# Kernel tuning notes

Hardware: AMD Instinct MI355X
Metric: run time of the kernel (lower is better)

The kernel has to match this reference:

```python
import jax, jax.numpy as jnp
import numpy as np

B, N, DIM, H, DH = 2, 1024, 1024, 8, 64
DI = H * DH  # 512
K = 4        # depthwise conv kernel
EPS = 1.1920929e-07  # float32 eps (torch RMSNorm default)


def setup_inputs() -> dict:
    key = jax.random.key(0)
    ks = jax.random.split(key, 12)
    s = lambda k, shape, sc=0.02: jax.random.normal(k, shape, jnp.float32) * sc
    return dict(
        x=jax.random.normal(ks[0], (B, N, DIM), jnp.float32),
        w_rms=jnp.ones((DIM,), jnp.float32),
        wq=s(ks[1], (DIM, DI)), wk=s(ks[2], (DIM, DI)), wv=s(ks[3], (DIM, DI)),
        wo=s(ks[4], (DI, DIM)),
        conv_q=s(ks[5], (DIM, K), 0.3), conv_k=s(ks[6], (DIM, K), 0.3), conv_v=s(ks[7], (DIM, K), 0.3),
        gamma_q=jnp.ones((H, 1, DH), jnp.float32), gamma_k=jnp.ones((H, 1, DH), jnp.float32),
        lr_w=s(ks[8], (DIM, H)), lr_b=jnp.full((H,), -4.0, jnp.float32),
        decay_w=s(ks[9], (DIM, H)), decay_b=jnp.full((H,), 4.0, jnp.float32),
        mom_w=s(ks[10], (DIM, H)), mom_b=jnp.full((H,), 2.0, jnp.float32),
    )


def rmsnorm(x, w):
    return x * jax.lax.rsqrt(jnp.mean(x * x, -1, keepdims=True) + EPS) * w


def mh_rmsnorm(x, gamma):  # x: (b, h, n, d)
    rms = jnp.sqrt(jnp.sum(x * x, -1, keepdims=True)) * (DH ** -0.5)
    return x / jnp.maximum(rms, 1e-8) * gamma


def dwconv(x, w):  # x: (b, n, dim), w: (dim, K) depthwise, padding K//2 -> length n+1
    y = jax.lax.conv_general_dilated(
        x.transpose(0, 2, 1), w[:, None, :], (1,), [(K // 2, K // 2)],
        feature_group_count=DIM, dimension_numbers=('NCW', 'OIW', 'NCW'))
    return y.transpose(0, 2, 1)


def gated_scan(a, x):  # h_t = a_t h_{t-1} + x_t, h_{-1}=0; a:(bh,t), x:(bh,t,d,d)
    def combine(c1, c2):
        a1, x1 = c1
        a2, x2 = c2
        return a1 * a2, a2 * x1 + x2
    _, h = jax.lax.associative_scan(combine, (a[..., None, None], x), axis=1)
    return h


def reference(x, w_rms, wq, wk, wv, wo, conv_q, conv_k, conv_v,
              gamma_q, gamma_k, lr_w, lr_b, decay_w, decay_b, mom_w, mom_b):
    b, n, _ = x.shape
    xa = rmsnorm(x, w_rms)
    qi, ki, vi = dwconv(xa, conv_q), dwconv(xa, conv_k), dwconv(xa, conv_v)
    split = lambda t: t.reshape(b, -1, H, DH).transpose(0, 2, 1, 3)[:, :, :n]  # (b,h,n,d)
    q = mh_rmsnorm(split(qi @ wq), gamma_q)
    k = mh_rmsnorm(split(ki @ wk), gamma_k)
    v = split(vi @ wv)
    fq = q.reshape(b * H, n, DH)
    fk = k.reshape(b * H, n, DH)
    fv = v.reshape(b * H, n, DH)
    sig = jax.nn.sigmoid
    lr = sig(xa @ lr_w + lr_b).transpose(0, 2, 1).reshape(b * H, n)
    decay = sig(xa @ decay_w + decay_b).transpose(0, 2, 1).reshape(b * H, n)
    mom = sig(xa @ mom_w + mom_b).transpose(0, 2, 1).reshape(b * H, n)
    # S_ref = S0 = 0 (fresh state) => pred = 0, delta_vec = -v
    g = jnp.einsum('bti,btj->btij', -fv, fk)          # (bh, n, d, d)
    Z = gated_scan(mom, g)                             # momentum scan
    S = gated_scan(decay, -lr[..., None, None] * Z)    # memory scan
    S_prev = jnp.concatenate([jnp.zeros_like(S[:, :1]), S[:, :-1]], axis=1)
    y = jnp.einsum('btdp,btp->btd', S_prev, fq)        # retrieval y_t = S_{t-1} psi_t
    y = y.reshape(b, H, n, DH).transpose(0, 2, 1, 3).reshape(b, n, DI)
    return y @ wo
```

## Files before the change

kernel.cpp:

```cpp
#include <hip/hip_runtime.h>
#include <math.h>

#define DEV __device__ __forceinline__

constexpr int Bb   = 2;
constexpr int Seq  = 1024;
constexpr int Dim  = 1024;
constexpr int Hh   = 8;
constexpr int Dh   = 64;
constexpr int Di   = 512;
constexpr int BN   = Bb * Seq;
constexpr int NSEQ = Bb * Hh;
constexpr int CHUNK = 32;
constexpr int CLEN  = Seq / CHUNK;
constexpr float EPSV = 1.1920929e-07f;
constexpr int NT2  = 8;
constexpr int KSPL = 8;

typedef _Float16 half8 __attribute__((ext_vector_type(8)));
typedef float    f32x4 __attribute__((ext_vector_type(4)));

DEV float bf2f(unsigned short u) {
  union { unsigned int i; float f; } x; x.i = ((unsigned int)u) << 16; return x.f;
}
DEV unsigned short f2bf(float f) {
  union { float f; unsigned int i; } x; x.f = f;
  unsigned int r = x.i + 0x7fffu + ((x.i >> 16) & 1u);
  return (unsigned short)(r >> 16);
}
DEV float ldin(const void* p, int f32, size_t i) {
  if (f32) return ((const float*)p)[i];
  return bf2f(((const unsigned short*)p)[i]);
}
DEV void ld4(const void* p, int f32, size_t i, float* dst) {
  if (f32) {
    float4 u = *(const float4*)((const float*)p + i);
    dst[0] = u.x; dst[1] = u.y; dst[2] = u.z; dst[3] = u.w;
  } else {
    ushort4 u = *(const ushort4*)((const unsigned short*)p + i);
    dst[0] = bf2f(u.x); dst[1] = bf2f(u.y); dst[2] = bf2f(u.z); dst[3] = bf2f(u.w);
  }
}
DEV int sniff_vote(const void* p, int n, int tid) {
  int j = 2 * tid, valid = 0, bad = 0;
  if (j < n) {
    valid = 1;
    float v = bf2f(((const unsigned short*)p)[j]);
    float a = fabsf(v);
    if (!(a >= 1e-12f && a <= 1e4f)) bad = 1;
  }
#pragma unroll
  for (int m = 1; m < 64; m <<= 1) { valid += __shfl_xor(valid, m); bad += __shfl_xor(bad, m); }
  return (2 * bad > valid) ? 1 : 0;
}

DEV void gld16(const _Float16* g, _Float16* l) {
  __builtin_amdgcn_global_load_lds(
      (const __attribute__((address_space(1))) void*)g,
      (__attribute__((address_space(3))) void*)l, 16, 0, 0);
}

struct InPtrs { const void* p[17]; int n[17]; };

__global__ __launch_bounds__(256) void k_front(
    InPtrs ip,
    int* __restrict__ flags,
    _Float16* __restrict__ wqT, _Float16* __restrict__ wkT,
    _Float16* __restrict__ wvT, _Float16* __restrict__ woT,
    _Float16* __restrict__ WgT,
    float* __restrict__ gqf, float* __restrict__ gkf, float* __restrict__ gbf,
    _Float16* __restrict__ xaf,
    _Float16* __restrict__ qc, _Float16* __restrict__ kc,
    _Float16* __restrict__ vc)
{
  int blk = blockIdx.x;
  int tid = threadIdx.x;
  __shared__ int sfl[8];
  __shared__ __align__(16) char smem_u[11 * Dim * 2];

  if (blk < 1024) {
    int z = blk >> 8, bx = blk & 15, by = (blk >> 4) & 15;
    int idx = (z == 0) ? 2 : ((z == 1) ? 3 : ((z == 2) ? 4 : 5));
    const void* src = ip.p[idx];
    _Float16* dst   = (z == 0) ? wqT : ((z == 1) ? wkT : ((z == 2) ? wvT : woT));
    int Kd = (z < 3) ? Dim : Di;
    int Nn = (z < 3) ? Di : Dim;
    int n0 = bx * 64, k0 = by * 64;
    if (n0 >= Nn || k0 >= Kd) return;

    if (tid < 64) { int f = sniff_vote(src, ip.n[idx], tid); if (tid == 0) sfl[0] = f; }
    __syncthreads();
    int f = sfl[0];

    float (*tile)[65] = (float(*)[65])smem_u;
    int r = tid >> 4, c4 = (tid & 15) * 4;
#pragma unroll
    for (int rr = 0; rr < 4; ++rr) {
      int k = rr * 16 + r;
      ld4(src, f, (size_t)(k0 + k) * Nn + n0 + c4, &tile[k][c4]);
    }
    __syncthreads();
#pragma unroll
    for (int rr = 0; rr < 4; ++rr) {
      int n = rr * 16 + r;
      _Float16 o4[4];
#pragma unroll
      for (int j = 0; j < 4; ++j) o4[j] = (_Float16)tile[c4 + j][n];
      *(ushort4*)&dst[(size_t)(n0 + n) * Kd + k0 + c4] = *(ushort4*)o4;
    }
  } else if (blk < 1088) {
    int row = blk - 1024;
    if (row < 24) {
      int g = row >> 3, h = row & 7;
      int idx = (g == 0) ? 11 : ((g == 1) ? 13 : 15);
      const void* W = ip.p[idx];
      if (tid < 64) { int f = sniff_vote(W, ip.n[idx], tid); if (tid == 0) sfl[0] = f; }
      __syncthreads();
      int f = sfl[0];
#pragma unroll
      for (int it = 0; it < 4; ++it) {
        int d = it * 256 + tid;
        WgT[(size_t)row * Dim + d] = (_Float16)ldin(W, f, (size_t)d * Hh + h);
      }
    } else {
#pragma unroll
      for (int it = 0; it < 4; ++it)
        WgT[(size_t)row * Dim + it * 256 + tid] = (_Float16)0.f;
    }
  } else if (blk == 1088) {
    __shared__ int allf[17];
    for (int ii = 0; ii < 17; ++ii) {
      if (tid < 64) {
        int f = sniff_vote(ip.p[ii], ip.n[ii], tid);
        if (tid == 0) { flags[ii] = f; allf[ii] = f; }
      }
    }
    __syncthreads();
    int f9 = allf[9], f10 = allf[10];
    for (int i = tid; i < Di; i += 256) {
      gqf[i] = ldin(ip.p[9], f9, i);
      gkf[i] = ldin(ip.p[10], f10, i);
    }
    if (tid < 24) {
      int g = tid >> 3, h = tid & 7;
      int idx = (g == 0) ? 12 : ((g == 1) ? 14 : 16);
      gbf[tid] = ldin(ip.p[idx], allf[idx], h);
    }
  } else {
    constexpr int NR = NT2 + 3;
    _Float16 (*xas)[Dim] = (_Float16(*)[Dim])smem_u;

    int rb = blk - 1089;
    int tb = rb & 127, b = rb >> 7;
    int t0 = tb * NT2;
    int lane = tid & 63, wv = tid >> 6;

    if (tid < 64) {
      int f0 = sniff_vote(ip.p[0], ip.n[0], tid);
      int f1 = sniff_vote(ip.p[1], ip.n[1], tid);
      int f6 = sniff_vote(ip.p[6], ip.n[6], tid);
      int f7 = sniff_vote(ip.p[7], ip.n[7], tid);
      int f8 = sniff_vote(ip.p[8], ip.n[8], tid);
      if (tid == 0) { sfl[0] = f0; sfl[1] = f1; sfl[2] = f6; sfl[3] = f7; sfl[4] = f8; }
    }
    __syncthreads();
    int fx = sfl[0], fw = sfl[1], f6 = sfl[2], f7 = sfl[3], f8 = sfl[4];
    int e0 = lane * 16;

    float wr[16];
#pragma unroll
    for (int q = 0; q < 4; ++q) ld4(ip.p[1], fw, e0 + q * 4, &wr[q * 4]);

    for (int rr = wv; rr < NR; rr += 4) {
      int r = t0 - 2 + rr;
      float xv[16];
      bool inr = (r >= 0 && r < Seq);
      if (inr) {
        size_t rbx = (size_t)(b * Seq + r) * Dim + e0;
#pragma unroll
        for (int q = 0; q < 4; ++q) ld4(ip.p[0], fx, rbx + q * 4, &xv[q * 4]);
      } else {
#pragma unroll
        for (int j = 0; j < 16; ++j) xv[j] = 0.f;
      }
      float ss = 0.f;
#pragma unroll
      for (int j = 0; j < 16; ++j) ss = fmaf(xv[j], xv[j], ss);
#pragma unroll
      for (int m = 1; m < 64; m <<= 1) ss += __shfl_xor(ss, m);
      float scale = rsqrtf(ss * (1.0f / Dim) + EPSV);

      _Float16 o[16];
#pragma unroll
      for (int j = 0; j < 16; ++j) o[j] = (_Float16)(xv[j] * scale * wr[j]);
      *(uint4*)&xas[rr][e0]     = *(uint4*)&o[0];
      *(uint4*)&xas[rr][e0 + 8] = *(uint4*)&o[8];
      if (inr && r >= t0 && r < t0 + NT2) {
        size_t ob = (size_t)(b * Seq + r) * Dim + e0;
        *(uint4*)&xaf[ob]     = *(uint4*)&o[0];
        *(uint4*)&xaf[ob + 8] = *(uint4*)&o[8];
      }
    }
    __syncthreads();

    int c0 = tid * 4;
    float lwq[16], lwk[16], lwv[16];
#pragma unroll
    for (int q = 0; q < 4; ++q) {
      ld4(ip.p[6], f6, (size_t)c0 * 4 + q * 4, &lwq[q * 4]);
      ld4(ip.p[7], f7, (size_t)c0 * 4 + q * 4, &lwk[q * 4]);
      ld4(ip.p[8], f8, (size_t)c0 * 4 + q * 4, &lwv[q * 4]);
    }

#pragma unroll
    for (int tt = 0; tt < NT2; ++tt) {
      float rv[4][4];
#pragma unroll
      for (int k = 0; k < 4; ++k) {
        _Float16 hx[4];
        *(ushort4*)hx = *(const ushort4*)&xas[tt + k][c0];
#pragma unroll
        for (int j = 0; j < 4; ++j) rv[k][j] = (float)hx[j];
      }
      _Float16 tq[4], tk[4], tv[4];
#pragma unroll
      for (int j = 0; j < 4; ++j) {
        float aq = rv[0][j] * lwq[j * 4 + 0] + rv[1][j] * lwq[j * 4 + 1]
                 + rv[2][j] * lwq[j * 4 + 2] + rv[3][j] * lwq[j * 4 + 3];
        float ak = rv[0][j] * lwk[j * 4 + 0] + rv[1][j] * lwk[j * 4 + 1]
                 + rv[2][j] * lwk[j * 4 + 2] + rv[3][j] * lwk[j * 4 + 3];
        float av = rv[0][j] * lwv[j * 4 + 0] + rv[1][j] * lwv[j * 4 + 1]
                 + rv[2][j] * lwv[j * 4 + 2] + rv[3][j] * lwv[j * 4 + 3];
        tq[j] = (_Float16)aq; tk[j] = (_Float16)ak; tv[j] = (_Float16)av;
      }
      size_t o = ((size_t)(b * Seq + t0 + tt)) * Dim + c0;
      *(ushort4*)&qc[o] = *(ushort4*)tq;
      *(ushort4*)&kc[o] = *(ushort4*)tk;
      *(ushort4*)&vc[o] = *(ushort4*)tv;
    }
  }
}

__global__ __launch_bounds__(256) void k_mid(
    const _Float16* __restrict__ qc, const _Float16* __restrict__ kc,
    const _Float16* __restrict__ vc,
    const _Float16* __restrict__ wqT, const _Float16* __restrict__ wkT,
    const _Float16* __restrict__ wvT,
    const _Float16* __restrict__ xaf, const _Float16* __restrict__ WgT,
    _Float16* __restrict__ qpre, _Float16* __restrict__ kpre,
    _Float16* __restrict__ vpre,
    float* __restrict__ gpart)
{
  __shared__ __align__(16) _Float16 ldsbuf[256 * 32];

  int blk = blockIdx.x;
  int tid = threadIdx.x, lane = tid & 63, wv = tid >> 6;
  int mrow = lane & 15, quad = lane >> 4;

  if (blk < 192) {
    int z = blk >> 6, rem = blk & 63;
    int by = rem >> 2, bx = rem & 3;
    const _Float16* A  = (z == 0) ? qc : ((z == 1) ? kc : vc);
    const _Float16* Bt = (z == 0) ? wqT : ((z == 1) ? wkT : wvT);
    _Float16* C        = (z == 0) ? qpre : ((z == 1) ? kpre : vpre);
    int m0 = by * 128, n0 = bx * 128;
    int wr = wv >> 1, wc = wv & 1;

    _Float16* Asl = ldsbuf;
    _Float16* Bsl = ldsbuf + 128 * 32;

    int sr = lane >> 2, sc = (lane & 3) * 8;

    f32x4 acc[4][4];
#pragma unroll
    for (int mi = 0; mi < 4; ++mi)
#pragma unroll
      for (int ni = 0; ni < 4; ++ni) acc[mi][ni] = (f32x4){0.f, 0.f, 0.f, 0.f};

    for (int kt = 0; kt < Dim; kt += 32) {
      __syncthreads();
      gld16(&A [(size_t)(m0 + wv * 32      + sr) * Dim + kt + sc], &Asl[(wv * 32     ) * 32]);
      gld16(&A [(size_t)(m0 + wv * 32 + 16 + sr) * Dim + kt + sc], &Asl[(wv * 32 + 16) * 32]);
      gld16(&Bt[(size_t)(n0 + wv * 32      + sr) * Dim + kt + sc], &Bsl[(wv * 32     ) * 32]);
      gld16(&Bt[(size_t)(n0 + wv * 32 + 16 + sr) * Dim + kt + sc], &Bsl[(wv * 32 + 16) * 32]);
      __syncthreads();

      half8 afr[4], bfr[4];
#pragma unroll
      for (int i = 0; i < 4; ++i)
        afr[i] = *(const half8*)&Asl[(wr * 64 + i * 16 + mrow) * 32 + quad * 8];
#pragma unroll
      for (int i = 0; i < 4; ++i)
        bfr[i] = *(const half8*)&Bsl[(wc * 64 + i * 16 + mrow) * 32 + quad * 8];
#pragma unroll
      for (int mi = 0; mi < 4; ++mi)
#pragma unroll
        for (int ni = 0; ni < 4; ++ni)
          acc[mi][ni] = __builtin_amdgcn_mfma_f32_16x16x32_f16(afr[mi], bfr[ni], acc[mi][ni], 0, 0, 0);
    }

#pragma unroll
    for (int mi = 0; mi < 4; ++mi) {
#pragma unroll
      for (int ni = 0; ni < 4; ++ni) {
        int col = n0 + wc * 64 + ni * 16 + mrow;
#pragma unroll
        for (int r2 = 0; r2 < 4; ++r2) {
          int row = m0 + wr * 64 + mi * 16 + quad * 4 + r2;
          C[(size_t)row * Di + col] = (_Float16)acc[mi][ni][r2];
        }
      }
    }
  } else {
    _Float16 (*As)[40] = (_Float16(*)[40])ldsbuf;
    _Float16 (*Bs)[40] = (_Float16(*)[40])(ldsbuf + 128 * 40);

    int g = blk - 192;
    int m0 = (g & 31) * 64, ks = g >> 5;
    int srow = tid >> 2, scol = (tid & 3) * 8;
    int kbase = ks * (Dim / KSPL);

    f32x4 acc[4];
#pragma unroll
    for (int mi = 0; mi < 4; ++mi) acc[mi] = (f32x4){0.f, 0.f, 0.f, 0.f};

    for (int kt = kbase; kt < kbase + Dim / KSPL; kt += 32) {
      __syncthreads();
      *(uint4*)&As[srow][scol] = *(const uint4*)&xaf[(size_t)(m0 + srow) * Dim + kt + scol];
      *(uint4*)&Bs[srow][scol] = *(const uint4*)&WgT[(size_t)srow * Dim + kt + scol];
      __syncthreads();
      half8 bfr = *(const half8*)&Bs[wv * 16 + mrow][quad * 8];
#pragma unroll
      for (int mi = 0; mi < 4; ++mi) {
        half8 afr = *(const half8*)&As[mi * 16 + mrow][quad * 8];
        acc[mi] = __builtin_amdgcn_mfma_f32_16x16x32_f16(afr, bfr, acc[mi], 0, 0, 0);
      }
    }

    int col = wv * 16 + mrow;
    if (col < 24) {
#pragma unroll
      for (int mi = 0; mi < 4; ++mi) {
#pragma unroll
        for (int r2 = 0; r2 < 4; ++r2) {
          int row = m0 + mi * 16 + quad * 4 + r2;
          gpart[((size_t)ks * BN + row) * 32 + col] = acc[mi][r2];
        }
      }
    }
  }
}

__global__ __launch_bounds__(256) void k_gemm_fin(
    const _Float16* __restrict__ A, const _Float16* __restrict__ Bt,
    void* __restrict__ C, const int* __restrict__ flags, int Nn, int Kd)
{
  __shared__ __align__(16) _Float16 lds[(128 + 64) * 32];
  _Float16* Asl = lds;
  _Float16* Bsl = lds + 128 * 32;

  int tid = threadIdx.x, lane = tid & 63, wv = tid >> 6;
  int n0 = blockIdx.x * 64, m0 = blockIdx.y * 128;
  int mrow = lane & 15, quad = lane >> 4;
  int wm = wv * 32;
  int sr = lane >> 2, sc = (lane & 3) * 8;

  f32x4 acc[2][4];
#pragma unroll
  for (int mi = 0; mi < 2; ++mi)
#pragma unroll
    for (int ni = 0; ni < 4; ++ni) acc[mi][ni] = (f32x4){0.f, 0.f, 0.f, 0.f};

  for (int kt = 0; kt < Kd; kt += 32) {
    __syncthreads();
    gld16(&A [(size_t)(m0 + wv * 32      + sr) * Kd + kt + sc], &Asl[(wv * 32     ) * 32]);
    gld16(&A [(size_t)(m0 + wv * 32 + 16 + sr) * Kd + kt + sc], &Asl[(wv * 32 + 16) * 32]);
    gld16(&Bt[(size_t)(n0 + wv * 16      + sr) * Kd + kt + sc], &Bsl[(wv * 16     ) * 32]);
    __syncthreads();

    half8 bfr[4];
#pragma unroll
    for (int ni = 0; ni < 4; ++ni)
      bfr[ni] = *(const half8*)&Bsl[(ni * 16 + mrow) * 32 + quad * 8];
#pragma unroll
    for (int mi = 0; mi < 2; ++mi) {
      half8 afr = *(const half8*)&Asl[(wm + mi * 16 + mrow) * 32 + quad * 8];
#pragma unroll
      for (int ni = 0; ni < 4; ++ni)
        acc[mi][ni] = __builtin_amdgcn_mfma_f32_16x16x32_f16(afr, bfr[ni], acc[mi][ni], 0, 0, 0);
    }
  }

  int any_bf16 = 0;
#pragma unroll
  for (int i2 = 0; i2 < 17; ++i2) any_bf16 |= (flags[i2] == 0);

#pragma unroll
  for (int mi = 0; mi < 2; ++mi) {
#pragma unroll
    for (int ni = 0; ni < 4; ++ni) {
      int col = n0 + ni * 16 + mrow;
#pragma unroll
      for (int r2 = 0; r2 < 4; ++r2) {
        int row = m0 + wm + mi * 16 + quad * 4 + r2;
        float v = acc[mi][ni][r2];
        size_t idx = (size_t)row * Nn + col;
        if (any_bf16) ((unsigned short*)C)[idx] = f2bf(v);
        else          ((float*)C)[idx] = v;
      }
    }
  }
}

DEV void load_gates(const float* __restrict__ gpart, const float* __restrict__ gbf,
                    int b, int h, int c, int tid,
                    float* gl, float* gd, float* gm)
{
  if (tid < 96) {
    int which = tid >> 5, t2 = tid & 31;
    int col = which * 8 + h;
    int row = b * Seq + c * CLEN + t2;
    float acc = gbf[col];
#pragma unroll
    for (int ks = 0; ks < KSPL; ++ks)
      acc += gpart[((size_t)ks * BN + row) * 32 + col];
    float sg = 1.f / (1.f + expf(-acc));
    if (which == 0) gl[t2] = sg; else if (which == 1) gd[t2] = sg; else gm[t2] = sg;
  }
}

__global__ __launch_bounds__(256) void k_phaseA(
    _Float16* __restrict__ kpre, const _Float16* __restrict__ vpre,
    const float* __restrict__ gkf,
    const float* __restrict__ gpart, const float* __restrict__ gbf,
    _Float16* __restrict__ ZS_Z, _Float16* __restrict__ ZS_S,
    float* __restrict__ Mc, float* __restrict__ Dc, float* __restrict__ Wc)
{
  int c = blockIdx.x, s = blockIdx.y;
  int b = s >> 3, h = s & 7;
  int tid = threadIdx.x, lane = tid & 63, wv = tid >> 6;
  int i = tid >> 2, j0 = (tid & 3) * 16;
  __shared__ float kn[CLEN][64], vv[CLEN][64];
  __shared__ float gl[CLEN], gd[CLEN], gm[CLEN];

  {
    int t = tid >> 3, col = (tid & 7) * 8;
    size_t g = ((size_t)(b * Seq + c * CLEN + t)) * Di + h * 64 + col;
    half8 kv = *(const half8*)&kpre[g];
    half8 vvv = *(const half8*)&vpre[g];
#pragma unroll
    for (int j = 0; j < 8; ++j) { kn[t][col + j] = (float)kv[j]; vv[t][col + j] = (float)vvv[j]; }
    load_gates(gpart, gbf, b, h, c, tid, gl, gd, gm);
  }
  __syncthreads();
  {
    float gk = gkf[h * 64 + lane];
#pragma unroll
    for (int tt = 0; tt < 8; ++tt) {
      int t = wv * 8 + tt;
      float kvv = kn[t][lane];
      float ss = kvv * kvv;
#pragma unroll
      for (int m = 1; m < 64; m <<= 1) ss += __shfl_xor(ss, m);
      float knv = kvv * (1.f / fmaxf(sqrtf(ss) * 0.125f, 1e-8f)) * gk;
      kn[t][lane] = knv;
      kpre[((size_t)(b * Seq + c * CLEN + t)) * Di + h * 64 + lane] = (_Float16)knv;
    }
  }
  __syncthreads();

  float Zl[16], Sl[16];
#pragma unroll
  for (int jj = 0; jj < 16; ++jj) { Zl[jj] = 0.f; Sl[jj] = 0.f; }
  float Mcum = 1.f, Dcum = 1.f, wacc = 0.f;

  for (int t = 0; t < CLEN; ++t) {
    float l = gl[t], dd = gd[t], mm = gm[t];
    float vi = vv[t][i];
    Mcum *= mm;
#pragma unroll
    for (int jj = 0; jj < 16; ++jj) {
      Zl[jj] = fmaf(mm, Zl[jj], -vi * kn[t][j0 + jj]);
      Sl[jj] = fmaf(dd, Sl[jj], -l * Zl[jj]);
    }
    wacc = fmaf(dd, wacc, -l * Mcum);
    Dcum *= dd;
  }
  size_t base = ((size_t)(s * CHUNK + c)) * 4096 + (size_t)i * 64 + j0;
  half8 zo0, zo1, so0, so1;
#pragma unroll
  for (int jj = 0; jj < 8; ++jj) {
    zo0[jj] = (_Float16)Zl[jj];     zo1[jj] = (_Float16)Zl[jj + 8];
    so0[jj] = (_Float16)Sl[jj];     so1[jj] = (_Float16)Sl[jj + 8];
  }
  *(half8*)&ZS_Z[base] = zo0; *(half8*)&ZS_Z[base + 8] = zo1;
  *(half8*)&ZS_S[base] = so0; *(half8*)&ZS_S[base + 8] = so1;
  if (tid == 0) {
    Mc[s * CHUNK + c] = Mcum; Dc[s * CHUNK + c] = Dcum; Wc[s * CHUNK + c] = wacc;
  }
}

__global__ __launch_bounds__(256) void k_phaseB(
    _Float16* __restrict__ ZS_Z, _Float16* __restrict__ ZS_S,
    const float* __restrict__ Mc, const float* __restrict__ Dc,
    const float* __restrict__ Wc)
{
  int s = blockIdx.x;
  int e = blockIdx.y * 256 + threadIdx.x;
  float Z = 0.f, S = 0.f;
  for (int c = 0; c < CHUNK; ++c) {
    size_t base = ((size_t)(s * CHUNK + c)) * 4096 + e;
    float mc = Mc[s * CHUNK + c], dc = Dc[s * CHUNK + c], wc = Wc[s * CHUNK + c];
    float zl = (float)ZS_Z[base], sl = (float)ZS_S[base];
    ZS_Z[base] = (_Float16)Z; ZS_S[base] = (_Float16)S;
    S = fmaf(dc, S, fmaf(wc, Z, sl));
    Z = fmaf(mc, Z, zl);
  }
}

__global__ __launch_bounds__(256) void k_phaseC(
    const _Float16* __restrict__ qpre, const _Float16* __restrict__ kpre,
    const _Float16* __restrict__ vpre,
    const float* __restrict__ gqf,
    const float* __restrict__ gpart, const float* __restrict__ gbf,
    const _Float16* __restrict__ ZS_Z, const _Float16* __restrict__ ZS_S,
    _Float16* __restrict__ yb)
{
  int c = blockIdx.x, s = blockIdx.y;
  int b = s >> 3, h = s & 7;
  int tid = threadIdx.x, lane = tid & 63, wv = tid >> 6;
  int i = tid >> 2, j0 = (tid & 3) * 16;
  __shared__ float kn[CLEN][64], vv[CLEN][64], qn[CLEN][64];
  __shared__ float gl[CLEN], gd[CLEN], gm[CLEN];

  float Zi_[16], Si_[16], Zl[16], Sl[16];
  size_t base = ((size_t)(s * CHUNK + c)) * 4096 + (size_t)i * 64 + j0;
  {
    half8 z0 = *(const half8*)&ZS_Z[base], z1 = *(const half8*)&ZS_Z[base + 8];
    half8 s0 = *(const half8*)&ZS_S[base], s1 = *(const half8*)&ZS_S[base + 8];
#pragma unroll
    for (int jj = 0; jj < 8; ++jj) {
      Zi_[jj] = (float)z0[jj]; Zi_[jj + 8] = (float)z1[jj];
      Si_[jj] = (float)s0[jj]; Si_[jj + 8] = (float)s1[jj];
      Zl[jj] = 0.f; Zl[jj + 8] = 0.f; Sl[jj] = 0.f; Sl[jj + 8] = 0.f;
    }
  }
  {
    int t = tid >> 3, col = (tid & 7) * 8;
    size_t g = ((size_t)(b * Seq + c * CLEN + t)) * Di + h * 64 + col;
    half8 kv = *(const half8*)&kpre[g];
    half8 vvv = *(const half8*)&vpre[g];
    half8 qv = *(const half8*)&qpre[g];
#pragma unroll
    for (int j = 0; j < 8; ++j) {
      kn[t][col + j] = (float)kv[j]; vv[t][col + j] = (float)vvv[j];
      qn[t][col + j] = (float)qv[j];
    }
    load_gates(gpart, gbf, b, h, c, tid, gl, gd, gm);
  }
  __syncthreads();
  {
    float gq = gqf[h * 64 + lane];
#pragma unroll
    for (int tt = 0; tt < 8; ++tt) {
      int t = wv * 8 + tt;
      float qvv = qn[t][lane];
      float ssq = qvv * qvv;
#pragma unroll
      for (int m = 1; m < 64; m <<= 1) ssq += __shfl_xor(ssq, m);
      qn[t][lane] = qvv * (1.f / fmaxf(sqrtf(ssq) * 0.125f, 1e-8f)) * gq;
    }
  }
  __syncthreads();

  float Mcum = 1.f, Dcum = 1.f, wacc = 0.f;
  float Dprev = 1.f, wprev = 0.f;

  for (int t = 0; t < CLEN; ++t) {
    float l = gl[t], dd = gd[t], mm = gm[t];

    float yp = 0.f;
#pragma unroll
    for (int jj = 0; jj < 16; ++jj) {
      float tmp = fmaf(Dprev, Si_[jj], fmaf(wprev, Zi_[jj], Sl[jj]));
      yp = fmaf(tmp, qn[t][j0 + jj], yp);
    }
    yp += __shfl_xor(yp, 1);
    yp += __shfl_xor(yp, 2);
    if ((tid & 3) == 0)
      yb[((size_t)(b * Seq + c * CLEN + t)) * Di + h * 64 + i] = (_Float16)yp;

    float vi = vv[t][i];
    Mcum *= mm;
#pragma unroll
    for (int jj = 0; jj < 16; ++jj) {
      Zl[jj] = fmaf(mm, Zl[jj], -vi * kn[t][j0 + jj]);
      Sl[jj] = fmaf(dd, Sl[jj], -l * Zl[jj]);
    }
    wacc = fmaf(dd, wacc, -l * Mcum);
    Dcum *= dd;
    Dprev = Dcum; wprev = wacc;
  }
}

extern "C" void kernel_launch(void* const* d_in, const int* in_sizes, int n_in,
                              void* d_out, int out_size, void* d_ws, size_t ws_size,
                              hipStream_t stream) {
  InPtrs ip;
  for (int i = 0; i < 17; ++i) { ip.p[i] = d_in[i]; ip.n[i] = in_sizes[i]; }

  char* p = (char*)d_ws;
  auto take = [&](size_t bytes) -> char* {
    char* q = p; p += (bytes + 255) & ~(size_t)255; return q;
  };
  int* flags           = (int*)take(32 * 4);
  _Float16* xaf        = (_Float16*)take((size_t)BN * Dim * 2);
  _Float16* qc         = (_Float16*)take((size_t)BN * Dim * 2);
  _Float16* kc         = (_Float16*)take((size_t)BN * Dim * 2);
  _Float16* vc         = (_Float16*)take((size_t)BN * Dim * 2);
  _Float16* qpre       = (_Float16*)take((size_t)BN * Di * 2);
  _Float16* kpre       = (_Float16*)take((size_t)BN * Di * 2);
  _Float16* vpre       = (_Float16*)take((size_t)BN * Di * 2);
  float* gpart         = (float*)take((size_t)KSPL * BN * 32 * 4);
  float* Mc            = (float*)take((size_t)NSEQ * CHUNK * 4);
  float* Dc            = (float*)take((size_t)NSEQ * CHUNK * 4);
  float* Wc            = (float*)take((size_t)NSEQ * CHUNK * 4);
  _Float16* wqT        = (_Float16*)take((size_t)Di * Dim * 2);
  _Float16* wkT        = (_Float16*)take((size_t)Di * Dim * 2);
  _Float16* wvT        = (_Float16*)take((size_t)Di * Dim * 2);
  _Float16* woT        = (_Float16*)take((size_t)Dim * Di * 2);
  _Float16* WgT        = (_Float16*)take((size_t)64 * Dim * 2);
  float* gqf           = (float*)take(Di * 4);
  float* gkf           = (float*)take(Di * 4);
  float* gbf           = (float*)take(32 * 4);
  _Float16* ZS_Z       = qc;
  _Float16* ZS_S       = kc;
  _Float16* yb         = vc;

  k_front<<<1345, 256, 0, stream>>>(ip, flags, wqT, wkT, wvT, woT, WgT,
                                    gqf, gkf, gbf, xaf, qc, kc, vc);

  k_mid<<<448, 256, 0, stream>>>(qc, kc, vc, wqT, wkT, wvT, xaf, WgT,
                                 qpre, kpre, vpre, gpart);

  k_phaseA<<<dim3(CHUNK, NSEQ), 256, 0, stream>>>(kpre, vpre, gkf,
                                                  gpart, gbf,
                                                  ZS_Z, ZS_S, Mc, Dc, Wc);
  k_phaseB<<<dim3(NSEQ, 16), 256, 0, stream>>>(ZS_Z, ZS_S, Mc, Dc, Wc);
  k_phaseC<<<dim3(CHUNK, NSEQ), 256, 0, stream>>>(qpre, kpre, vpre, gqf,
                                                  gpart, gbf,
                                                  ZS_Z, ZS_S, yb);

  k_gemm_fin<<<dim3(Dim / 64, BN / 128), 256, 0, stream>>>(
      yb, woT, d_out, flags, Dim, Di);
}
```

Before: 181.0 us.

## Compute intra-chunk retrieval in phase A and shrink phase C to inter-chunk term

Phase A now also normalizes q and computes the intra-chunk retrieval contribution and the per-step coefficients (Dprev, wprev), storing them to new workspace buffers. Phase C then only loads the normalized q and the carried-in states, adding the inter-chunk terms, instead of recomputing the whole local Z/S recurrence. This removes the duplicated recurrence and the k/v loads from phase C, at the cost of extra fp32 traffic for the ub buffer. Separately, the QKV projection GEMM switches from 128x128 to 128x64 tiles, doubling block count for better occupancy across CUs.

```diff
diff --git a/kernel.cpp b/kernel.cpp
--- a/kernel.cpp
+++ b/kernel.cpp
@@ -241,6 +241,56 @@
   }
 }
 
+DEV void gemm_tile_12864_f16(
+    const _Float16* __restrict__ A, const _Float16* __restrict__ Bt,
+    _Float16* __restrict__ C, int Nn, int Kd, int m0, int n0,
+    _Float16* Asl, _Float16* Bsl, int tid)
+{
+  int lane = tid & 63, wv = tid >> 6;
+  int mrow = lane & 15, quad = lane >> 4;
+  int wm = wv * 32;
+  int sr = lane >> 2, sc = (lane & 3) * 8;
+
+  f32x4 acc[2][4];
+#pragma unroll
+  for (int mi = 0; mi < 2; ++mi)
+#pragma unroll
+    for (int ni = 0; ni < 4; ++ni) acc[mi][ni] = (f32x4){0.f, 0.f, 0.f, 0.f};
+
+  for (int kt = 0; kt < Kd; kt += 32) {
+    __syncthreads();
+    gld16(&A [(size_t)(m0 + wv * 32      + sr) * Kd + kt + sc], &Asl[(wv * 32     ) * 32]);
+    gld16(&A [(size_t)(m0 + wv * 32 + 16 + sr) * Kd + kt + sc], &Asl[(wv * 32 + 16) * 32]);
+    gld16(&Bt[(size_t)(n0 + wv * 16      + sr) * Kd + kt + sc], &Bsl[(wv * 16     ) * 32]);
+    __syncthreads();
+
+    half8 bfr[4];
+#pragma unroll
+    for (int ni = 0; ni < 4; ++ni)
+      bfr[ni] = *(const half8*)&Bsl[(ni * 16 + mrow) * 32 + quad * 8];
+#pragma unroll
+    for (int mi = 0; mi < 2; ++mi) {
+      half8 afr = *(const half8*)&Asl[(wm + mi * 16 + mrow) * 32 + quad * 8];
+#pragma unroll
+      for (int ni = 0; ni < 4; ++ni)
+        acc[mi][ni] = __builtin_amdgcn_mfma_f32_16x16x32_f16(afr, bfr[ni], acc[mi][ni], 0, 0, 0);
+    }
+  }
+
+#pragma unroll
+  for (int mi = 0; mi < 2; ++mi) {
+#pragma unroll
+    for (int ni = 0; ni < 4; ++ni) {
+      int col = n0 + ni * 16 + mrow;
+#pragma unroll
+      for (int r2 = 0; r2 < 4; ++r2) {
+        int row = m0 + wm + mi * 16 + quad * 4 + r2;
+        C[(size_t)row * Nn + col] = (_Float16)acc[mi][ni][r2];
+      }
+    }
+  }
+}
+
 __global__ __launch_bounds__(256) void k_mid(
     const _Float16* __restrict__ qc, const _Float16* __restrict__ kc,
     const _Float16* __restrict__ vc,
@@ -257,65 +307,19 @@
   int tid = threadIdx.x, lane = tid & 63, wv = tid >> 6;
   int mrow = lane & 15, quad = lane >> 4;
 
-  if (blk < 192) {
-    int z = blk >> 6, rem = blk & 63;
-    int by = rem >> 2, bx = rem & 3;
+  if (blk < 384) {
+    int z = blk >> 7, rem = blk & 127;
+    int by = rem >> 3, bx = rem & 7;
     const _Float16* A  = (z == 0) ? qc : ((z == 1) ? kc : vc);
     const _Float16* Bt = (z == 0) ? wqT : ((z == 1) ? wkT : wvT);
     _Float16* C        = (z == 0) ? qpre : ((z == 1) ? kpre : vpre);
-    int m0 = by * 128, n0 = bx * 128;
-    int wr = wv >> 1, wc = wv & 1;
-
-    _Float16* Asl = ldsbuf;
-    _Float16* Bsl = ldsbuf + 128 * 32;
-
-    int sr = lane >> 2, sc = (lane & 3) * 8;
-
-    f32x4 acc[4][4];
-#pragma unroll
-    for (int mi = 0; mi < 4; ++mi)
-#pragma unroll
-      for (int ni = 0; ni < 4; ++ni) acc[mi][ni] = (f32x4){0.f, 0.f, 0.f, 0.f};
-
-    for (int kt = 0; kt < Dim; kt += 32) {
-      __syncthreads();
-      gld16(&A [(size_t)(m0 + wv * 32      + sr) * Dim + kt + sc], &Asl[(wv * 32     ) * 32]);
-      gld16(&A [(size_t)(m0 + wv * 32 + 16 + sr) * Dim + kt + sc], &Asl[(wv * 32 + 16) * 32]);
-      gld16(&Bt[(size_t)(n0 + wv * 32      + sr) * Dim + kt + sc], &Bsl[(wv * 32     ) * 32]);
-      gld16(&Bt[(size_t)(n0 + wv * 32 + 16 + sr) * Dim + kt + sc], &Bsl[(wv * 32 + 16) * 32]);
-      __syncthreads();
-
-      half8 afr[4], bfr[4];
-#pragma unroll
-      for (int i = 0; i < 4; ++i)
-        afr[i] = *(const half8*)&Asl[(wr * 64 + i * 16 + mrow) * 32 + quad * 8];
-#pragma unroll
-      for (int i = 0; i < 4; ++i)
-        bfr[i] = *(const half8*)&Bsl[(wc * 64 + i * 16 + mrow) * 32 + quad * 8];
-#pragma unroll
-      for (int mi = 0; mi < 4; ++mi)
-#pragma unroll
-        for (int ni = 0; ni < 4; ++ni)
-          acc[mi][ni] = __builtin_amdgcn_mfma_f32_16x16x32_f16(afr[mi], bfr[ni], acc[mi][ni], 0, 0, 0);
-    }
-
-#pragma unroll
-    for (int mi = 0; mi < 4; ++mi) {
-#pragma unroll
-      for (int ni = 0; ni < 4; ++ni) {
-        int col = n0 + wc * 64 + ni * 16 + mrow;
-#pragma unroll
-        for (int r2 = 0; r2 < 4; ++r2) {
-          int row = m0 + wr * 64 + mi * 16 + quad * 4 + r2;
-          C[(size_t)row * Di + col] = (_Float16)acc[mi][ni][r2];
-        }
-      }
-    }
+    gemm_tile_12864_f16(A, Bt, C, Di, Dim, by * 128, bx * 64,
+                        ldsbuf, ldsbuf + 128 * 32, tid);
   } else {
     _Float16 (*As)[40] = (_Float16(*)[40])ldsbuf;
     _Float16 (*Bs)[40] = (_Float16(*)[40])(ldsbuf + 128 * 40);
 
-    int g = blk - 192;
+    int g = blk - 384;
     int m0 = (g & 31) * 64, ks = g >> 5;
     int srow = tid >> 2, scol = (tid & 3) * 8;
     int kbase = ks * (Dim / KSPL);
@@ -430,17 +434,20 @@
 }
 
 __global__ __launch_bounds__(256) void k_phaseA(
-    _Float16* __restrict__ kpre, const _Float16* __restrict__ vpre,
-    const float* __restrict__ gkf,
+    const _Float16* __restrict__ kpre, const _Float16* __restrict__ vpre,
+    _Float16* __restrict__ qpre,
+    const float* __restrict__ gkf, const float* __restrict__ gqf,
     const float* __restrict__ gpart, const float* __restrict__ gbf,
     _Float16* __restrict__ ZS_Z, _Float16* __restrict__ ZS_S,
-    float* __restrict__ Mc, float* __restrict__ Dc, float* __restrict__ Wc)
+    float* __restrict__ Mc, float* __restrict__ Dc, float* __restrict__ Wc,
+    float* __restrict__ ub, float* __restrict__ ab)
 {
   int c = blockIdx.x, s = blockIdx.y;
   int b = s >> 3, h = s & 7;
   int tid = threadIdx.x, lane = tid & 63, wv = tid >> 6;
   int i = tid >> 2, j0 = (tid & 3) * 16;
-  __shared__ float kn[CLEN][64], vv[CLEN][64];
+  int sc_ = s * CHUNK + c;
+  __shared__ float kn[CLEN][64], vv[CLEN][64], qn[CLEN][64];
   __shared__ float gl[CLEN], gd[CLEN], gm[CLEN];
 
   {
@@ -448,23 +455,31 @@
     size_t g = ((size_t)(b * Seq + c * CLEN + t)) * Di + h * 64 + col;
     half8 kv = *(const half8*)&kpre[g];
     half8 vvv = *(const half8*)&vpre[g];
-#pragma unroll
-    for (int j = 0; j < 8; ++j) { kn[t][col + j] = (float)kv[j]; vv[t][col + j] = (float)vvv[j]; }
+    half8 qv = *(const half8*)&qpre[g];
+#pragma unroll
+    for (int j = 0; j < 8; ++j) {
+      kn[t][col + j] = (float)kv[j]; vv[t][col + j] = (float)vvv[j];
+      qn[t][col + j] = (float)qv[j];
+    }
     load_gates(gpart, gbf, b, h, c, tid, gl, gd, gm);
   }
   __syncthreads();
   {
     float gk = gkf[h * 64 + lane];
+    float gq = gqf[h * 64 + lane];
 #pragma unroll
     for (int tt = 0; tt < 8; ++tt) {
       int t = wv * 8 + tt;
       float kvv = kn[t][lane];
-      float ss = kvv * kvv;
-#pragma unroll
-      for (int m = 1; m < 64; m <<= 1) ss += __shfl_xor(ss, m);
-      float knv = kvv * (1.f / fmaxf(sqrtf(ss) * 0.125f, 1e-8f)) * gk;
-      kn[t][lane] = knv;
-      kpre[((size_t)(b * Seq + c * CLEN + t)) * Di + h * 64 + lane] = (_Float16)knv;
+      float ssk = kvv * kvv;
+      float qvv = qn[t][lane];
+      float ssq = qvv * qvv;
+#pragma unroll
+      for (int m = 1; m < 64; m <<= 1) { ssk += __shfl_xor(ssk, m); ssq += __shfl_xor(ssq, m); }
+      kn[t][lane] = kvv * (1.f / fmaxf(sqrtf(ssk) * 0.125f, 1e-8f)) * gk;
+      float qnv = qvv * (1.f / fmaxf(sqrtf(ssq) * 0.125f, 1e-8f)) * gq;
+      qn[t][lane] = qnv;
+      qpre[((size_t)(b * Seq + c * CLEN + t)) * Di + h * 64 + lane] = (_Float16)qnv;
     }
   }
   __syncthreads();
@@ -473,9 +488,21 @@
 #pragma unroll
   for (int jj = 0; jj < 16; ++jj) { Zl[jj] = 0.f; Sl[jj] = 0.f; }
   float Mcum = 1.f, Dcum = 1.f, wacc = 0.f;
+  float Dprev = 1.f, wprev = 0.f;
 
   for (int t = 0; t < CLEN; ++t) {
     float l = gl[t], dd = gd[t], mm = gm[t];
+
+    float up = 0.f;
+#pragma unroll
+    for (int jj = 0; jj < 16; ++jj)
+      up = fmaf(Sl[jj], qn[t][j0 + jj], up);
+    up += __shfl_xor(up, 1);
+    up += __shfl_xor(up, 2);
+    if ((tid & 3) == 0) ub[((size_t)sc_ * CLEN + t) * 64 + i] = up;
+    if (tid == 0) ab[(size_t)sc_ * 64 + t * 2]     = Dprev;
+    if (tid == 1) ab[(size_t)sc_ * 64 + t * 2 + 1] = wprev;
+
     float vi = vv[t][i];
     Mcum *= mm;
 #pragma unroll
@@ -485,8 +512,9 @@
     }
     wacc = fmaf(dd, wacc, -l * Mcum);
     Dcum *= dd;
-  }
-  size_t base = ((size_t)(s * CHUNK + c)) * 4096 + (size_t)i * 64 + j0;
+    Dprev = Dcum; wprev = wacc;
+  }
+  size_t base = ((size_t)sc_) * 4096 + (size_t)i * 64 + j0;
   half8 zo0, zo1, so0, so1;
 #pragma unroll
   for (int jj = 0; jj < 8; ++jj) {
@@ -496,7 +524,7 @@
   *(half8*)&ZS_Z[base] = zo0; *(half8*)&ZS_Z[base + 8] = zo1;
   *(half8*)&ZS_S[base] = so0; *(half8*)&ZS_S[base + 8] = so1;
   if (tid == 0) {
-    Mc[s * CHUNK + c] = Mcum; Dc[s * CHUNK + c] = Dcum; Wc[s * CHUNK + c] = wacc;
+    Mc[sc_] = Mcum; Dc[sc_] = Dcum; Wc[sc_] = wacc;
   }
 }
 
@@ -519,22 +547,21 @@
 }
 
 __global__ __launch_bounds__(256) void k_phaseC(
-    const _Float16* __restrict__ qpre, const _Float16* __restrict__ kpre,
-    const _Float16* __restrict__ vpre,
-    const float* __restrict__ gqf,
-    const float* __restrict__ gpart, const float* __restrict__ gbf,
+    const _Float16* __restrict__ qpre,
     const _Float16* __restrict__ ZS_Z, const _Float16* __restrict__ ZS_S,
+    const float* __restrict__ ub, const float* __restrict__ ab,
     _Float16* __restrict__ yb)
 {
   int c = blockIdx.x, s = blockIdx.y;
   int b = s >> 3, h = s & 7;
-  int tid = threadIdx.x, lane = tid & 63, wv = tid >> 6;
+  int tid = threadIdx.x;
   int i = tid >> 2, j0 = (tid & 3) * 16;
-  __shared__ float kn[CLEN][64], vv[CLEN][64], qn[CLEN][64];
-  __shared__ float gl[CLEN], gd[CLEN], gm[CLEN];
-
-  float Zi_[16], Si_[16], Zl[16], Sl[16];
-  size_t base = ((size_t)(s * CHUNK + c)) * 4096 + (size_t)i * 64 + j0;
+  int sc_ = s * CHUNK + c;
+  __shared__ float qn[CLEN][64];
+  __shared__ float abs_[64];
+
+  float Zi_[16], Si_[16];
+  size_t base = ((size_t)sc_) * 4096 + (size_t)i * 64 + j0;
   {
     half8 z0 = *(const half8*)&ZS_Z[base], z1 = *(const half8*)&ZS_Z[base + 8];
     half8 s0 = *(const half8*)&ZS_S[base], s1 = *(const half8*)&ZS_S[base + 8];
@@ -542,64 +569,33 @@
     for (int jj = 0; jj < 8; ++jj) {
       Zi_[jj] = (float)z0[jj]; Zi_[jj + 8] = (float)z1[jj];
       Si_[jj] = (float)s0[jj]; Si_[jj + 8] = (float)s1[jj];
-      Zl[jj] = 0.f; Zl[jj + 8] = 0.f; Sl[jj] = 0.f; Sl[jj + 8] = 0.f;
     }
   }
   {
     int t = tid >> 3, col = (tid & 7) * 8;
     size_t g = ((size_t)(b * Seq + c * CLEN + t)) * Di + h * 64 + col;
-    half8 kv = *(const half8*)&kpre[g];
-    half8 vvv = *(const half8*)&vpre[g];
     half8 qv = *(const half8*)&qpre[g];
 #pragma unroll
-    for (int j = 0; j < 8; ++j) {
-      kn[t][col + j] = (float)kv[j]; vv[t][col + j] = (float)vvv[j];
-      qn[t][col + j] = (float)qv[j];
-    }
-    load_gates(gpart, gbf, b, h, c, tid, gl, gd, gm);
+    for (int j = 0; j < 8; ++j) qn[t][col + j] = (float)qv[j];
+    if (tid < 64) abs_[tid] = ab[(size_t)sc_ * 64 + tid];
   }
   __syncthreads();
-  {
-    float gq = gqf[h * 64 + lane];
-#pragma unroll
-    for (int tt = 0; tt < 8; ++tt) {
-      int t = wv * 8 + tt;
-      float qvv = qn[t][lane];
-      float ssq = qvv * qvv;
-#pragma unroll
-      for (int m = 1; m < 64; m <<= 1) ssq += __shfl_xor(ssq, m);
-      qn[t][lane] = qvv * (1.f / fmaxf(sqrtf(ssq) * 0.125f, 1e-8f)) * gq;
-    }
-  }
-  __syncthreads();
-
-  float Mcum = 1.f, Dcum = 1.f, wacc = 0.f;
-  float Dprev = 1.f, wprev = 0.f;
 
   for (int t = 0; t < CLEN; ++t) {
-    float l = gl[t], dd = gd[t], mm = gm[t];
-
-    float yp = 0.f;
+    float sq = 0.f, zq = 0.f;
 #pragma unroll
     for (int jj = 0; jj < 16; ++jj) {
-      float tmp = fmaf(Dprev, Si_[jj], fmaf(wprev, Zi_[jj], Sl[jj]));
-      yp = fmaf(tmp, qn[t][j0 + jj], yp);
-    }
-    yp += __shfl_xor(yp, 1);
-    yp += __shfl_xor(yp, 2);
-    if ((tid & 3) == 0)
-      yb[((size_t)(b * Seq + c * CLEN + t)) * Di + h * 64 + i] = (_Float16)yp;
-
-    float vi = vv[t][i];
-    Mcum *= mm;
-#pragma unroll
-    for (int jj = 0; jj < 16; ++jj) {
-      Zl[jj] = fmaf(mm, Zl[jj], -vi * kn[t][j0 + jj]);
-      Sl[jj] = fmaf(dd, Sl[jj], -l * Zl[jj]);
-    }
-    wacc = fmaf(dd, wacc, -l * Mcum);
-    Dcum *= dd;
-    Dprev = Dcum; wprev = wacc;
+      float q = qn[t][j0 + jj];
+      sq = fmaf(Si_[jj], q, sq);
+      zq = fmaf(Zi_[jj], q, zq);
+    }
+    sq += __shfl_xor(sq, 1); sq += __shfl_xor(sq, 2);
+    zq += __shfl_xor(zq, 1); zq += __shfl_xor(zq, 2);
+    if ((tid & 3) == 0) {
+      float a = abs_[t * 2], bb2 = abs_[t * 2 + 1];
+      float y = ub[((size_t)sc_ * CLEN + t) * 64 + i] + a * sq + bb2 * zq;
+      yb[((size_t)(b * Seq + c * CLEN + t)) * Di + h * 64 + i] = (_Float16)y;
+    }
   }
 }
 
@@ -625,6 +621,8 @@
   float* Mc            = (float*)take((size_t)NSEQ * CHUNK * 4);
   float* Dc            = (float*)take((size_t)NSEQ * CHUNK * 4);
   float* Wc            = (float*)take((size_t)NSEQ * CHUNK * 4);
+  float* ub            = (float*)take((size_t)NSEQ * CHUNK * CLEN * 64 * 4);
+  float* ab            = (float*)take((size_t)NSEQ * CHUNK * 64 * 4);
   _Float16* wqT        = (_Float16*)take((size_t)Di * Dim * 2);
   _Float16* wkT        = (_Float16*)take((size_t)Di * Dim * 2);
   _Float16* wvT        = (_Float16*)take((size_t)Di * Dim * 2);
@@ -640,16 +638,15 @@
   k_front<<<1345, 256, 0, stream>>>(ip, flags, wqT, wkT, wvT, woT, WgT,
                                     gqf, gkf, gbf, xaf, qc, kc, vc);
 
-  k_mid<<<448, 256, 0, stream>>>(qc, kc, vc, wqT, wkT, wvT, xaf, WgT,
+  k_mid<<<640, 256, 0, stream>>>(qc, kc, vc, wqT, wkT, wvT, xaf, WgT,
                                  qpre, kpre, vpre, gpart);
 
-  k_phaseA<<<dim3(CHUNK, NSEQ), 256, 0, stream>>>(kpre, vpre, gkf,
+  k_phaseA<<<dim3(CHUNK, NSEQ), 256, 0, stream>>>(kpre, vpre, qpre, gkf, gqf,
                                                   gpart, gbf,
-                                                  ZS_Z, ZS_S, Mc, Dc, Wc);
+                                                  ZS_Z, ZS_S, Mc, Dc, Wc,
+                                                  ub, ab);
   k_phaseB<<<dim3(NSEQ, 16), 256, 0, stream>>>(ZS_Z, ZS_S, Mc, Dc, Wc);
-  k_phaseC<<<dim3(CHUNK, NSEQ), 256, 0, stream>>>(qpre, kpre, vpre, gqf,
-                                                  gpart, gbf,
-                                                  ZS_Z, ZS_S, yb);
+  k_phaseC<<<dim3(CHUNK, NSEQ), 256, 0, stream>>>(qpre, ZS_Z, ZS_S, ub, ab, yb);
 
   k_gemm_fin<<<dim3(Dim / 64, BN / 128), 256, 0, stream>>>(
       yb, woT, d_out, flags, Dim, Di);
```

Measured after the change: 185.9 us. 1.03x slower.
